# Performance work log

Hardware: AMD Instinct MI355X
Metric: run time of the kernel (lower is better)

Reference implementation:

```python
import jax, jax.numpy as jnp
import numpy as np

N, T, K, R, DK = 4096, 8, 4, 8, 64
S = 2   # slot_dim (2D coords)
B = 20  # noise samples (hardcoded in original forward)


def _conv1d(x, w, b, pad):
    # x: [batch, Cin, L], w: [Cout, Cin, ks] (torch Conv1d layout == OIH)
    y = jax.lax.conv_general_dilated(x, w, (1,), [(pad, pad)],
                                     dimension_numbers=('NCH', 'OIH', 'NCH'))
    return y + b[None, :, None]


def setup_inputs() -> dict:
    key = jax.random.key(0)
    ks = iter(jax.random.split(key, 40))
    r = lambda shape, s=0.1: jax.random.normal(next(ks), shape, jnp.float32) * s
    return dict(
        obs=r((1, S, N, T), 1.0),
        obs_vel=r((1, S, N, T), 1.0),
        noise=r((B, 2, 1, 1), 1.0),
        wq_rule=r((S * T, DK)), bq_rule=r((DK,)),
        wq_ctx=r((2 * S * T, DK)), bq_ctx=r((DK,)),
        wk_ctx=r((2 * S * T, DK)), bk_ctx=r((DK,)),
        rule_emb=r((R, DK), 1.0),
        w_noise=r((R,), 1.0), w_indiv=r((R,), 1.0), w_social=r((R,), 1.0),
        sp_w=r((R, S, S * (K + 1), 3)), sp_b=r((R, S)),
        spr_w=r((R, S, S * (K + 1), 1)), spr_b=r((R, S)),
        tp_w=r((R, 12, T, 3)), tp_b=r((R, 12)),
        tpr_w=r((R, 12, T, 1)), tpr_b=r((R, 12)),
        spi_w=r((R, S, S, 3)), spi_b=r((R, S)),
        spir_w=r((R, S, S, 1)), spir_b=r((R, S)),
        tpi_w=r((R, 12, T, 3)), tpi_b=r((R, 12)),
        tpir_w=r((R, 12, T, 1)), tpir_b=r((R, 12)),
    )


def reference(obs, obs_vel, noise, wq_rule, bq_rule, wq_ctx, bq_ctx, wk_ctx, bk_ctx,
              rule_emb, w_noise, w_indiv, w_social,
              sp_w, sp_b, spr_w, spr_b, tp_w, tp_b, tpr_w, tpr_b,
              spi_w, spi_b, spir_w, spir_b, tpi_w, tpi_b, tpir_w, tpir_b):
    # ---- context selection (eval path: topk_onehot) ----
    cat = jnp.concatenate([obs, obs_vel], axis=1)[0]           # [2S, N, T]
    x_ctx = jnp.transpose(cat, (1, 2, 0)).reshape(N, -1)       # [N, T*2S]
    q = x_ctx @ wq_ctx + bq_ctx
    k_ = x_ctx @ wk_ctx + bk_ctx
    attn_ctx = jax.nn.softmax(q @ k_.T, axis=-1)               # [N, N]
    _, ctx_idx = jax.lax.top_k(attn_ctx, K)                    # [N, K]
    # gather == bmm with one-hot [N,N] masks in the original
    ov_node = jnp.transpose(obs_vel[0], (1, 0, 2))             # [N, S, T]
    ctx_vel = ov_node[ctx_idx]                                 # [N, K, S, T]
    ctx_vel = jnp.transpose(ctx_vel, (1, 2, 0, 3)).reshape(1, K * S, N, T)

    # ---- rule selection (hard top-1) ----
    x_rule = jnp.transpose(obs_vel[0], (1, 2, 0)).reshape(N, -1)  # [N, T*S]
    rq = x_rule @ wq_rule + bq_rule
    attn_rule = jax.nn.softmax(rq @ rule_emb.T, axis=-1)       # [N, R]
    rule_mask = jax.nn.one_hot(jnp.argmax(attn_rule, -1), R, dtype=obs.dtype)  # [N, R]

    noise_rep = jnp.tile(noise, (1, K, 1, 1))                  # [B, K*S, 1, 1]

    def rule_fn(wn, wi, ws, p):
        ov = obs_vel + noise * wn                              # [B, S, N, T]
        ov_f = jnp.transpose(ov, (0, 2, 1, 3)).reshape(B * N, S, T)
        cv = ctx_vel + noise_rep * wn                          # [B, K*S, N, T]
        cv_f = jnp.transpose(cv, (0, 2, 1, 3)).reshape(B * N, K * S, T)
        comb = jnp.concatenate([ov_f, cv_f], axis=1)           # [B*N, S*(K+1), T]
        si = jax.nn.relu(_conv1d(ov_f, p['spi_w'], p['spi_b'], 1)) \
             + _conv1d(ov_f, p['spir_w'], p['spir_b'], 0)      # [B*N, S, T]
        ti = jnp.transpose(si, (0, 2, 1))                      # [B*N, T, S]
        indiv = _conv1d(ti, p['tpi_w'], p['tpi_b'], 1) + _conv1d(ti, p['tpir_w'], p['tpir_b'], 0)
        ss = jax.nn.relu(_conv1d(comb, p['sp_w'], p['sp_b'], 1)) \
             + _conv1d(comb, p['spr_w'], p['spr_b'], 0)        # [B*N, S, T]
        ts = jnp.transpose(ss, (0, 2, 1))
        social = _conv1d(ts, p['tp_w'], p['tp_b'], 1) + _conv1d(ts, p['tpr_w'], p['tpr_b'], 0)
        return wi * indiv + ws * social                        # [B*N, 12, S]

    params = dict(sp_w=sp_w, sp_b=sp_b, spr_w=spr_w, spr_b=spr_b,
                  tp_w=tp_w, tp_b=tp_b, tpr_w=tpr_w, tpr_b=tpr_b,
                  spi_w=spi_w, spi_b=spi_b, spir_w=spir_w, spir_b=spir_b,
                  tpi_w=tpi_w, tpi_b=tpi_b, tpir_w=tpir_w, tpir_b=tpir_b)
    preds = jax.vmap(rule_fn)(w_noise, w_indiv, w_social, params)  # [R, B*N, 12, S]
    preds = preds.reshape(R, B, N, 12, S)
    # hard rule dispatch + final permute(0,2,3,1) of the original -> [B, N, 12, S]
    return jnp.einsum('rbnts,nr->bnts', preds, rule_mask)
```

## Files before the change

kernel.cpp:

```cpp
#include <hip/hip_runtime.h>
#include <cstdint>
#include <cstddef>

#define N_   4096
#define T_   8
#define K_   4
#define R_   8
#define DK_  64
#define S_   2
#define B_   20
#define NT_  (N_*T_)

__device__ __forceinline__ unsigned long long mkkey(float v, int col) {
    unsigned u = __float_as_uint(v);
    u = (u & 0x80000000u) ? ~u : (u | 0x80000000u);
    return ((unsigned long long)u << 32) | (unsigned)(~col);
}

#define INS4(t0,t1,t2,t3,keyexpr) do {                                  \
    unsigned long long _k = (keyexpr);                                  \
    if (_k > (t3)) {                                                    \
        bool _g2 = _k > (t2), _g1 = _k > (t1), _g0 = _k > (t0);         \
        (t3) = _g2 ? (t2) : _k;                                         \
        (t2) = _g2 ? (_g1 ? (t1) : _k) : (t2);                          \
        (t1) = _g1 ? (_g0 ? (t0) : _k) : (t1);                          \
        (t0) = _g0 ? _k : (t0);                                         \
    }                                                                   \
} while (0)

__device__ __forceinline__ unsigned long long shfl_xor_u64(unsigned long long v, int m) {
    unsigned lo = (unsigned)v, hi = (unsigned)(v >> 32);
    lo = __shfl_xor(lo, m, 64);
    hi = __shfl_xor(hi, m, 64);
    return ((unsigned long long)hi << 32) | lo;
}

__global__ __launch_bounds__(256) void proj_kernel(
    const float* __restrict__ obs, const float* __restrict__ obsv,
    const float* __restrict__ wq_ctx, const float* __restrict__ bq_ctx,
    const float* __restrict__ wk_ctx, const float* __restrict__ bk_ctx,
    const float* __restrict__ wq_rule, const float* __restrict__ bq_rule,
    const float* __restrict__ rule_emb,
    float* __restrict__ qg, float* __restrict__ kg, int* __restrict__ rid)
{
    int wv = threadIdx.x >> 6, d = threadIdx.x & 63;
    int n = blockIdx.x * 4 + wv;
    __shared__ float xs[4][32];
    if (d < 32) {
        int t = d >> 2, c = d & 3;
        const float* src = (c < 2) ? obs : obsv;
        xs[wv][d] = src[(c & 1) * NT_ + n * T_ + t];
    }
    __syncthreads();
    const float* x = xs[wv];
    float q = bq_ctx[d], k = bk_ctx[d], rq = bq_rule[d];
    #pragma unroll
    for (int i = 0; i < 32; ++i) {
        float xv = x[i];
        q = fmaf(xv, wq_ctx[i*64 + d], q);
        k = fmaf(xv, wk_ctx[i*64 + d], k);
    }
    #pragma unroll
    for (int i = 0; i < 16; ++i) {
        int t = i >> 1, s = i & 1;
        rq = fmaf(x[t*4 + 2 + s], wq_rule[i*64 + d], rq);
    }
    qg[n*64 + d] = q;
    kg[n*64 + d] = k;

    float best = -1e30f; int bestr = 0;
    #pragma unroll
    for (int r = 0; r < 8; ++r) {
        float p = rq * rule_emb[r*64 + d];
        #pragma unroll
        for (int off = 32; off > 0; off >>= 1) p += __shfl_xor(p, off, 64);
        if (p > best) { best = p; bestr = r; }
    }
    if (d == 0) rid[n] = bestr;
}

#define RPB     64
#define CTILE   64
#define NSPLIT  16
#define DPAD    68

__global__ __launch_bounds__(256) void attn_topk_kernel(
    const float* __restrict__ qg, const float* __restrict__ kg,
    unsigned long long* __restrict__ part)
{
    __shared__ float qT[DK_*DPAD];
    __shared__ float kT[DK_*DPAD];

    int tid = threadIdx.x;
    int tx = tid & 15, ty = tid >> 4;
    int rowblk = blockIdx.x >> 4, split = blockIdx.x & 15;
    int row0 = rowblk * RPB;
    int colbase = split * (N_ / NSPLIT);

    #pragma unroll
    for (int i = 0; i < 4; ++i) {
        int chunk = tid + 256*i;
        int row = chunk & 63, dchunk = chunk >> 6;
        float4 v = *(const float4*)(qg + (size_t)(row0 + row)*64 + 4*dchunk);
        qT[(4*dchunk+0)*DPAD + row] = v.x;
        qT[(4*dchunk+1)*DPAD + row] = v.y;
        qT[(4*dchunk+2)*DPAD + row] = v.z;
        qT[(4*dchunk+3)*DPAD + row] = v.w;
    }

    unsigned long long T0a=0,T0b=0,T0c=0,T0d=0;
    unsigned long long T1a=0,T1b=0,T1c=0,T1d=0;
    unsigned long long T2a=0,T2b=0,T2c=0,T2d=0;
    unsigned long long T3a=0,T3b=0,T3c=0,T3d=0;

    for (int tile = 0; tile < (N_/NSPLIT)/CTILE; ++tile) {
        int c0 = colbase + tile * CTILE;
        __syncthreads();
        #pragma unroll
        for (int i = 0; i < 4; ++i) {
            int chunk = tid + 256*i;
            int col = chunk & 63, dchunk = chunk >> 6;
            float4 v = *(const float4*)(kg + (size_t)(c0 + col)*64 + 4*dchunk);
            kT[(4*dchunk+0)*DPAD + col] = v.x;
            kT[(4*dchunk+1)*DPAD + col] = v.y;
            kT[(4*dchunk+2)*DPAD + col] = v.z;
            kT[(4*dchunk+3)*DPAD + col] = v.w;
        }
        __syncthreads();

        float c00=0,c01=0,c02=0,c03=0, c10=0,c11=0,c12=0,c13=0;
        float c20=0,c21=0,c22=0,c23=0, c30=0,c31=0,c32=0,c33=0;

        #pragma unroll 4
        for (int d = 0; d < 64; ++d) {
            float4 a = *(const float4*)(&qT[d*DPAD + 4*ty]);
            float4 b = *(const float4*)(&kT[d*DPAD + 4*tx]);
            c00 = fmaf(a.x, b.x, c00); c01 = fmaf(a.x, b.y, c01);
            c02 = fmaf(a.x, b.z, c02); c03 = fmaf(a.x, b.w, c03);
            c10 = fmaf(a.y, b.x, c10); c11 = fmaf(a.y, b.y, c11);
            c12 = fmaf(a.y, b.z, c12); c13 = fmaf(a.y, b.w, c13);
            c20 = fmaf(a.z, b.x, c20); c21 = fmaf(a.z, b.y, c21);
            c22 = fmaf(a.z, b.z, c22); c23 = fmaf(a.z, b.w, c23);
            c30 = fmaf(a.w, b.x, c30); c31 = fmaf(a.w, b.y, c31);
            c32 = fmaf(a.w, b.z, c32); c33 = fmaf(a.w, b.w, c33);
        }
        int cc = c0 + 4*tx;
        INS4(T0a,T0b,T0c,T0d, mkkey(c00, cc+0));
        INS4(T0a,T0b,T0c,T0d, mkkey(c01, cc+1));
        INS4(T0a,T0b,T0c,T0d, mkkey(c02, cc+2));
        INS4(T0a,T0b,T0c,T0d, mkkey(c03, cc+3));
        INS4(T1a,T1b,T1c,T1d, mkkey(c10, cc+0));
        INS4(T1a,T1b,T1c,T1d, mkkey(c11, cc+1));
        INS4(T1a,T1b,T1c,T1d, mkkey(c12, cc+2));
        INS4(T1a,T1b,T1c,T1d, mkkey(c13, cc+3));
        INS4(T2a,T2b,T2c,T2d, mkkey(c20, cc+0));
        INS4(T2a,T2b,T2c,T2d, mkkey(c21, cc+1));
        INS4(T2a,T2b,T2c,T2d, mkkey(c22, cc+2));
        INS4(T2a,T2b,T2c,T2d, mkkey(c23, cc+3));
        INS4(T3a,T3b,T3c,T3d, mkkey(c30, cc+0));
        INS4(T3a,T3b,T3c,T3d, mkkey(c31, cc+1));
        INS4(T3a,T3b,T3c,T3d, mkkey(c32, cc+2));
        INS4(T3a,T3b,T3c,T3d, mkkey(c33, cc+3));
    }

    #pragma unroll
    for (int m = 1; m < 16; m <<= 1) {
        unsigned long long r0, r1, r2, r3;
        r0 = shfl_xor_u64(T0a, m); r1 = shfl_xor_u64(T0b, m);
        r2 = shfl_xor_u64(T0c, m); r3 = shfl_xor_u64(T0d, m);
        INS4(T0a,T0b,T0c,T0d, r0); INS4(T0a,T0b,T0c,T0d, r1);
        INS4(T0a,T0b,T0c,T0d, r2); INS4(T0a,T0b,T0c,T0d, r3);
        r0 = shfl_xor_u64(T1a, m); r1 = shfl_xor_u64(T1b, m);
        r2 = shfl_xor_u64(T1c, m); r3 = shfl_xor_u64(T1d, m);
        INS4(T1a,T1b,T1c,T1d, r0); INS4(T1a,T1b,T1c,T1d, r1);
        INS4(T1a,T1b,T1c,T1d, r2); INS4(T1a,T1b,T1c,T1d, r3);
        r0 = shfl_xor_u64(T2a, m); r1 = shfl_xor_u64(T2b, m);
        r2 = shfl_xor_u64(T2c, m); r3 = shfl_xor_u64(T2d, m);
        INS4(T2a,T2b,T2c,T2d, r0); INS4(T2a,T2b,T2c,T2d, r1);
        INS4(T2a,T2b,T2c,T2d, r2); INS4(T2a,T2b,T2c,T2d, r3);
        r0 = shfl_xor_u64(T3a, m); r1 = shfl_xor_u64(T3b, m);
        r2 = shfl_xor_u64(T3c, m); r3 = shfl_xor_u64(T3d, m);
        INS4(T3a,T3b,T3c,T3d, r0); INS4(T3a,T3b,T3c,T3d, r1);
        INS4(T3a,T3b,T3c,T3d, r2); INS4(T3a,T3b,T3c,T3d, r3);
    }

    if (tx == 0) {
        unsigned long long* q;
        q = &part[(size_t)((row0 + 4*ty + 0)*NSPLIT + split)*4];
        q[0]=T0a; q[1]=T0b; q[2]=T0c; q[3]=T0d;
        q = &part[(size_t)((row0 + 4*ty + 1)*NSPLIT + split)*4];
        q[0]=T1a; q[1]=T1b; q[2]=T1c; q[3]=T1d;
        q = &part[(size_t)((row0 + 4*ty + 2)*NSPLIT + split)*4];
        q[0]=T2a; q[1]=T2b; q[2]=T2c; q[3]=T2d;
        q = &part[(size_t)((row0 + 4*ty + 3)*NSPLIT + split)*4];
        q[0]=T3a; q[1]=T3b; q[2]=T3c; q[3]=T3d;
    }
}

__global__ __launch_bounds__(256) void merge_kernel(
    const unsigned long long* __restrict__ part, int* __restrict__ cidx)
{
    int n = blockIdx.x * blockDim.x + threadIdx.x;
    if (n >= N_) return;
    unsigned long long m0=0,m1=0,m2=0,m3=0;
    #pragma unroll 8
    for (int j = 0; j < NSPLIT*4; ++j) INS4(m0,m1,m2,m3, part[(size_t)n*NSPLIT*4 + j]);
    cidx[n*4 + 0] = (int)(~((unsigned)(m0 & 0xffffffffull)));
    cidx[n*4 + 1] = (int)(~((unsigned)(m1 & 0xffffffffull)));
    cidx[n*4 + 2] = (int)(~((unsigned)(m2 & 0xffffffffull)));
    cidx[n*4 + 3] = (int)(~((unsigned)(m3 & 0xffffffffull)));
}

#define WST 708

__global__ __launch_bounds__(256) void predict_kernel(
    const float* __restrict__ obsv, const float* __restrict__ noise,
    const float* __restrict__ w_noise, const float* __restrict__ w_indiv,
    const float* __restrict__ w_social,
    const float* __restrict__ sp_w, const float* __restrict__ sp_b,
    const float* __restrict__ spr_w, const float* __restrict__ spr_b,
    const float* __restrict__ tp_w, const float* __restrict__ tp_b,
    const float* __restrict__ tpr_w, const float* __restrict__ tpr_b,
    const float* __restrict__ spi_w, const float* __restrict__ spi_b,
    const float* __restrict__ spir_w, const float* __restrict__ spir_b,
    const float* __restrict__ tpi_w, const float* __restrict__ tpi_b,
    const float* __restrict__ tpir_w, const float* __restrict__ tpir_b,
    const int* __restrict__ rid, const int* __restrict__ cidx,
    float* __restrict__ out)
{
    __shared__ float W[R_*WST];
    __shared__ float nz_s[B_*2];
    __shared__ float wn_s[R_], wi_s[R_], ws_s[R_];
    int tid = threadIdx.x;

    for (int idx = tid; idx < R_*704; idx += 256) {
        int r = idx / 704, o = idx % 704;
        float v;
        if (o < 12)      v = spi_w[r*12 + o];
        else if (o < 16) v = spir_w[r*4 + (o-12)];
        else if (o < 76) v = sp_w[r*60 + (o-16)];
        else if (o < 96) v = spr_w[r*20 + (o-76)];
        else if (o < 192) { int q=o-96;  int t=q/12, co=q%12; v = tpi_w[((r*12+co)*8+t)*3+1] + tpir_w[(r*12+co)*8+t]; }
        else if (o < 288) { int q=o-192; int t=q/12, co=q%12; v = tpi_w[((r*12+co)*8+t)*3+2]; }
        else if (o < 384) { int q=o-288; int t=q/12, co=q%12; v = tpi_w[((r*12+co)*8+t)*3+0]; }
        else if (o < 480) { int q=o-384; int t=q/12, co=q%12; v = tp_w[((r*12+co)*8+t)*3+1] + tpr_w[(r*12+co)*8+t]; }
        else if (o < 576) { int q=o-480; int t=q/12, co=q%12; v = tp_w[((r*12+co)*8+t)*3+2]; }
        else if (o < 672) { int q=o-576; int t=q/12, co=q%12; v = tp_w[((r*12+co)*8+t)*3+0]; }
        else if (o < 674) v = spi_b[r*2 + (o-672)];
        else if (o < 676) v = spir_b[r*2 + (o-674)];
        else if (o < 678) v = sp_b[r*2 + (o-676)];
        else if (o < 680) v = spr_b[r*2 + (o-678)];
        else if (o < 692) v = tpi_b[r*12 + (o-680)] + tpir_b[r*12 + (o-680)];
        else              v = tp_b[r*12 + (o-692)] + tpr_b[r*12 + (o-692)];
        W[r*WST + o] = v;
    }
    if (tid < B_*2)                  nz_s[tid] = noise[tid];
    if (tid >= 64  && tid < 64+R_)   wn_s[tid-64]  = w_noise[tid-64];
    if (tid >= 96  && tid < 96+R_)   wi_s[tid-96]  = w_indiv[tid-96];
    if (tid >= 128 && tid < 128+R_)  ws_s[tid-128] = w_social[tid-128];
    __syncthreads();

    int item = blockIdx.x*256 + tid;
    if (item >= B_*N_) return;
    int n = item / B_, b = item - n*B_;
    int r = rid[n];
    const float* Wr = &W[r*WST];
    float wn = wn_s[r];
    float nz0 = nz_s[b*2+0]*wn, nz1 = nz_s[b*2+1]*wn;

    float x[10][8];
    #pragma unroll
    for (int s = 0; s < 2; ++s) {
        float4 a = *(const float4*)(obsv + s*NT_ + n*8);
        float4 c = *(const float4*)(obsv + s*NT_ + n*8 + 4);
        float nz = s ? nz1 : nz0;
        x[s][0]=a.x+nz; x[s][1]=a.y+nz; x[s][2]=a.z+nz; x[s][3]=a.w+nz;
        x[s][4]=c.x+nz; x[s][5]=c.y+nz; x[s][6]=c.z+nz; x[s][7]=c.w+nz;
    }
    #pragma unroll
    for (int k = 0; k < 4; ++k) {
        int cn = cidx[n*4 + k];
        #pragma unroll
        for (int s = 0; s < 2; ++s) {
            float4 a = *(const float4*)(obsv + s*NT_ + cn*8);
            float4 c = *(const float4*)(obsv + s*NT_ + cn*8 + 4);
            float nz = s ? nz1 : nz0;
            int ch = 2 + k*2 + s;
            x[ch][0]=a.x+nz; x[ch][1]=a.y+nz; x[ch][2]=a.z+nz; x[ch][3]=a.w+nz;
            x[ch][4]=c.x+nz; x[ch][5]=c.y+nz; x[ch][6]=c.z+nz; x[ch][7]=c.w+nz;
        }
    }

    float si[2][8];
    #pragma unroll
    for (int so = 0; so < 2; ++so) {
        float pre[8];
        float bb = Wr[672+so];
        #pragma unroll
        for (int t = 0; t < 8; ++t) pre[t] = bb;
        #pragma unroll
        for (int ci = 0; ci < 2; ++ci) {
            float w0 = Wr[so*6+ci*3+0], w1 = Wr[so*6+ci*3+1], w2 = Wr[so*6+ci*3+2];
            pre[0] += x[ci][0]*w1 + x[ci][1]*w2;
            #pragma unroll
            for (int t = 1; t < 7; ++t) pre[t] += x[ci][t-1]*w0 + x[ci][t]*w1 + x[ci][t+1]*w2;
            pre[7] += x[ci][6]*w0 + x[ci][7]*w1;
        }
        float l0 = Wr[12+so*2+0], l1 = Wr[12+so*2+1];
        float lb = Wr[674+so];
        #pragma unroll
        for (int t = 0; t < 8; ++t)
            si[so][t] = fmaxf(pre[t], 0.f) + lb + x[0][t]*l0 + x[1][t]*l1;
    }

    float ss[2][8];
    #pragma unroll
    for (int so = 0; so < 2; ++so) {
        float pre[8], lin[8];
        float bb = Wr[676+so], lb = Wr[678+so];
        #pragma unroll
        for (int t = 0; t < 8; ++t) { pre[t] = bb; lin[t] = lb; }
        #pragma unroll
        for (int ci = 0; ci < 10; ++ci) {
            float w0 = Wr[16+so*30+ci*3+0], w1 = Wr[16+so*30+ci*3+1], w2 = Wr[16+so*30+ci*3+2];
            float lw = Wr[76+so*10+ci];
            pre[0] += x[ci][0]*w1 + x[ci][1]*w2;
            #pragma unroll
            for (int t = 1; t < 7; ++t) pre[t] += x[ci][t-1]*w0 + x[ci][t]*w1 + x[ci][t+1]*w2;
            pre[7] += x[ci][6]*w0 + x[ci][7]*w1;
            #pragma unroll
            for (int t = 0; t < 8; ++t) lin[t] += x[ci][t]*lw;
        }
        #pragma unroll
        for (int t = 0; t < 8; ++t) ss[so][t] = fmaxf(pre[t], 0.f) + lin[t];
    }

    float i0[12], i1[12], s0a[12], s1a[12];
    #pragma unroll
    for (int co = 0; co < 12; ++co) {
        float bi = Wr[680+co], bs = Wr[692+co];
        i0[co]=bi; i1[co]=bi; s0a[co]=bs; s1a[co]=bs;
    }
    #pragma unroll
    for (int t = 0; t < 8; ++t) {
        float a0 = si[0][t], a1 = si[1][t];
        float b0 = ss[0][t], b1 = ss[1][t];
        #pragma unroll
        for (int co = 0; co < 12; ++co) {
            i0[co]  += a0*Wr[96 +t*12+co] + a1*Wr[192+t*12+co];
            i1[co]  += a1*Wr[96 +t*12+co] + a0*Wr[288+t*12+co];
            s0a[co] += b0*Wr[384+t*12+co] + b1*Wr[480+t*12+co];
            s1a[co] += b1*Wr[384+t*12+co] + b0*Wr[576+t*12+co];
        }
    }

    float wi = wi_s[r], wsoc = ws_s[r];
    float o[24];
    #pragma unroll
    for (int co = 0; co < 12; ++co) {
        o[co*2+0] = wi*i0[co] + wsoc*s0a[co];
        o[co*2+1] = wi*i1[co] + wsoc*s1a[co];
    }
    float* dst = out + (size_t)(b*N_ + n)*24;
    #pragma unroll
    for (int q4 = 0; q4 < 6; ++q4)
        *(float4*)(dst + q4*4) = *(const float4*)(&o[q4*4]);
}

extern "C" void kernel_launch(void* const* d_in, const int* in_sizes, int n_in,
                              void* d_out, int out_size, void* d_ws, size_t ws_size,
                              hipStream_t stream)
{
    const float* obs      = (const float*)d_in[0];
    const float* obsv     = (const float*)d_in[1];
    const float* noise    = (const float*)d_in[2];
    const float* wq_rule  = (const float*)d_in[3];
    const float* bq_rule  = (const float*)d_in[4];
    const float* wq_ctx   = (const float*)d_in[5];
    const float* bq_ctx   = (const float*)d_in[6];
    const float* wk_ctx   = (const float*)d_in[7];
    const float* bk_ctx   = (const float*)d_in[8];
    const float* rule_emb = (const float*)d_in[9];
    const float* w_noise  = (const float*)d_in[10];
    const float* w_indiv  = (const float*)d_in[11];
    const float* w_social = (const float*)d_in[12];
    const float* sp_w  = (const float*)d_in[13];
    const float* sp_b  = (const float*)d_in[14];
    const float* spr_w = (const float*)d_in[15];
    const float* spr_b = (const float*)d_in[16];
    const float* tp_w  = (const float*)d_in[17];
    const float* tp_b  = (const float*)d_in[18];
    const float* tpr_w = (const float*)d_in[19];
    const float* tpr_b = (const float*)d_in[20];
    const float* spi_w  = (const float*)d_in[21];
    const float* spi_b  = (const float*)d_in[22];
    const float* spir_w = (const float*)d_in[23];
    const float* spir_b = (const float*)d_in[24];
    const float* tpi_w  = (const float*)d_in[25];
    const float* tpi_b  = (const float*)d_in[26];
    const float* tpir_w = (const float*)d_in[27];
    const float* tpir_b = (const float*)d_in[28];

    char* ws = (char*)d_ws;
    float* qg = (float*)(ws);
    float* kg = (float*)(ws + 1048576);
    unsigned long long* part = (unsigned long long*)(ws + 2097152);
    int* rid  = (int*)(ws + 4194304);
    int* cidx = (int*)(ws + 4210688);

    hipLaunchKernelGGL(proj_kernel, dim3(N_/4), dim3(256), 0, stream,
        obs, obsv, wq_ctx, bq_ctx, wk_ctx, bk_ctx, wq_rule, bq_rule, rule_emb,
        qg, kg, rid);

    hipLaunchKernelGGL(attn_topk_kernel, dim3((N_/RPB)*NSPLIT), dim3(256), 0, stream,
        qg, kg, part);

    hipLaunchKernelGGL(merge_kernel, dim3(N_/256), dim3(256), 0, stream,
        part, cidx);

    hipLaunchKernelGGL(predict_kernel, dim3((B_*N_)/256), dim3(256), 0, stream,
        obsv, noise, w_noise, w_indiv, w_social,
        sp_w, sp_b, spr_w, spr_b, tp_w, tp_b, tpr_w, tpr_b,
        spi_w, spi_b, spir_w, spir_b, tpi_w, tpi_b, tpir_w, tpir_b,
        rid, cidx, (float*)d_out);
}
```

Measured before the change: 213.9 us.

## Widen attention tile to 4x8 per thread and prepack rule weights once

Result: faster. 204.4 us (-4.4%).

```diff
diff --git a/kernel.cpp b/kernel.cpp
--- a/kernel.cpp
+++ b/kernel.cpp
@@ -80,32 +80,33 @@
 }
 
 #define RPB     64
-#define CTILE   64
-#define NSPLIT  16
-#define DPAD    68
+#define CTILE   128
+#define NSPLIT  8
+#define QST     68
+#define KST2    132
 
 __global__ __launch_bounds__(256) void attn_topk_kernel(
     const float* __restrict__ qg, const float* __restrict__ kg,
     unsigned long long* __restrict__ part)
 {
-    __shared__ float qT[DK_*DPAD];
-    __shared__ float kT[DK_*DPAD];
+    __shared__ float qT[DK_*QST];
+    __shared__ float kT[DK_*KST2];
 
     int tid = threadIdx.x;
     int tx = tid & 15, ty = tid >> 4;
-    int rowblk = blockIdx.x >> 4, split = blockIdx.x & 15;
+    int rowblk = blockIdx.x >> 3, split = blockIdx.x & 7;
     int row0 = rowblk * RPB;
     int colbase = split * (N_ / NSPLIT);
 
     #pragma unroll
     for (int i = 0; i < 4; ++i) {
         int chunk = tid + 256*i;
-        int row = chunk & 63, dchunk = chunk >> 6;
-        float4 v = *(const float4*)(qg + (size_t)(row0 + row)*64 + 4*dchunk);
-        qT[(4*dchunk+0)*DPAD + row] = v.x;
-        qT[(4*dchunk+1)*DPAD + row] = v.y;
-        qT[(4*dchunk+2)*DPAD + row] = v.z;
-        qT[(4*dchunk+3)*DPAD + row] = v.w;
+        int row = chunk & 63, dc = chunk >> 6;
+        float4 v = *(const float4*)(qg + (size_t)(row0 + row)*64 + 4*dc);
+        qT[(4*dc+0)*QST + row] = v.x;
+        qT[(4*dc+1)*QST + row] = v.y;
+        qT[(4*dc+2)*QST + row] = v.z;
+        qT[(4*dc+3)*QST + row] = v.w;
     }
 
     unsigned long long T0a=0,T0b=0,T0c=0,T0d=0;
@@ -117,50 +118,52 @@
         int c0 = colbase + tile * CTILE;
         __syncthreads();
         #pragma unroll
-        for (int i = 0; i < 4; ++i) {
+        for (int i = 0; i < 8; ++i) {
             int chunk = tid + 256*i;
-            int col = chunk & 63, dchunk = chunk >> 6;
-            float4 v = *(const float4*)(kg + (size_t)(c0 + col)*64 + 4*dchunk);
-            kT[(4*dchunk+0)*DPAD + col] = v.x;
-            kT[(4*dchunk+1)*DPAD + col] = v.y;
-            kT[(4*dchunk+2)*DPAD + col] = v.z;
-            kT[(4*dchunk+3)*DPAD + col] = v.w;
+            int col = chunk & 127, dc = chunk >> 7;
+            float4 v = *(const float4*)(kg + (size_t)(c0 + col)*64 + 4*dc);
+            kT[(4*dc+0)*KST2 + col] = v.x;
+            kT[(4*dc+1)*KST2 + col] = v.y;
+            kT[(4*dc+2)*KST2 + col] = v.z;
+            kT[(4*dc+3)*KST2 + col] = v.w;
         }
         __syncthreads();
 
-        float c00=0,c01=0,c02=0,c03=0, c10=0,c11=0,c12=0,c13=0;
-        float c20=0,c21=0,c22=0,c23=0, c30=0,c31=0,c32=0,c33=0;
-
-        #pragma unroll 4
+        float acc[4][8];
+        #pragma unroll
+        for (int i = 0; i < 4; ++i)
+            #pragma unroll
+            for (int j = 0; j < 8; ++j) acc[i][j] = 0.f;
+
+        #pragma unroll 2
         for (int d = 0; d < 64; ++d) {
-            float4 a = *(const float4*)(&qT[d*DPAD + 4*ty]);
-            float4 b = *(const float4*)(&kT[d*DPAD + 4*tx]);
-            c00 = fmaf(a.x, b.x, c00); c01 = fmaf(a.x, b.y, c01);
-            c02 = fmaf(a.x, b.z, c02); c03 = fmaf(a.x, b.w, c03);
-            c10 = fmaf(a.y, b.x, c10); c11 = fmaf(a.y, b.y, c11);
-            c12 = fmaf(a.y, b.z, c12); c13 = fmaf(a.y, b.w, c13);
-            c20 = fmaf(a.z, b.x, c20); c21 = fmaf(a.z, b.y, c21);
-            c22 = fmaf(a.z, b.z, c22); c23 = fmaf(a.z, b.w, c23);
-            c30 = fmaf(a.w, b.x, c30); c31 = fmaf(a.w, b.y, c31);
-            c32 = fmaf(a.w, b.z, c32); c33 = fmaf(a.w, b.w, c33);
-        }
-        int cc = c0 + 4*tx;
-        INS4(T0a,T0b,T0c,T0d, mkkey(c00, cc+0));
-        INS4(T0a,T0b,T0c,T0d, mkkey(c01, cc+1));
-        INS4(T0a,T0b,T0c,T0d, mkkey(c02, cc+2));
-        INS4(T0a,T0b,T0c,T0d, mkkey(c03, cc+3));
-        INS4(T1a,T1b,T1c,T1d, mkkey(c10, cc+0));
-        INS4(T1a,T1b,T1c,T1d, mkkey(c11, cc+1));
-        INS4(T1a,T1b,T1c,T1d, mkkey(c12, cc+2));
-        INS4(T1a,T1b,T1c,T1d, mkkey(c13, cc+3));
-        INS4(T2a,T2b,T2c,T2d, mkkey(c20, cc+0));
-        INS4(T2a,T2b,T2c,T2d, mkkey(c21, cc+1));
-        INS4(T2a,T2b,T2c,T2d, mkkey(c22, cc+2));
-        INS4(T2a,T2b,T2c,T2d, mkkey(c23, cc+3));
-        INS4(T3a,T3b,T3c,T3d, mkkey(c30, cc+0));
-        INS4(T3a,T3b,T3c,T3d, mkkey(c31, cc+1));
-        INS4(T3a,T3b,T3c,T3d, mkkey(c32, cc+2));
-        INS4(T3a,T3b,T3c,T3d, mkkey(c33, cc+3));
+            float4 a  = *(const float4*)(&qT[d*QST + 4*ty]);
+            float4 b0 = *(const float4*)(&kT[d*KST2 + 4*tx]);
+            float4 b1 = *(const float4*)(&kT[d*KST2 + 64 + 4*tx]);
+            float av[4] = {a.x, a.y, a.z, a.w};
+            float bv[8] = {b0.x, b0.y, b0.z, b0.w, b1.x, b1.y, b1.z, b1.w};
+            #pragma unroll
+            for (int i = 0; i < 4; ++i)
+                #pragma unroll
+                for (int j = 0; j < 8; ++j)
+                    acc[i][j] = fmaf(av[i], bv[j], acc[i][j]);
+        }
+        int ccA = c0 + 4*tx, ccB = c0 + 64 + 4*tx;
+        #define ROW8(t0,t1,t2,t3,i) do {                         \
+            INS4(t0,t1,t2,t3, mkkey(acc[i][0], ccA+0));          \
+            INS4(t0,t1,t2,t3, mkkey(acc[i][1], ccA+1));          \
+            INS4(t0,t1,t2,t3, mkkey(acc[i][2], ccA+2));          \
+            INS4(t0,t1,t2,t3, mkkey(acc[i][3], ccA+3));          \
+            INS4(t0,t1,t2,t3, mkkey(acc[i][4], ccB+0));          \
+            INS4(t0,t1,t2,t3, mkkey(acc[i][5], ccB+1));          \
+            INS4(t0,t1,t2,t3, mkkey(acc[i][6], ccB+2));          \
+            INS4(t0,t1,t2,t3, mkkey(acc[i][7], ccB+3));          \
+        } while (0)
+        ROW8(T0a,T0b,T0c,T0d, 0);
+        ROW8(T1a,T1b,T1c,T1d, 1);
+        ROW8(T2a,T2b,T2c,T2d, 2);
+        ROW8(T3a,T3b,T3c,T3d, 3);
+        #undef ROW8
     }
 
     #pragma unroll
@@ -213,10 +216,7 @@
 
 #define WST 708
 
-__global__ __launch_bounds__(256) void predict_kernel(
-    const float* __restrict__ obsv, const float* __restrict__ noise,
-    const float* __restrict__ w_noise, const float* __restrict__ w_indiv,
-    const float* __restrict__ w_social,
+__global__ __launch_bounds__(256) void prep_kernel(
     const float* __restrict__ sp_w, const float* __restrict__ sp_b,
     const float* __restrict__ spr_w, const float* __restrict__ spr_b,
     const float* __restrict__ tp_w, const float* __restrict__ tp_b,
@@ -225,16 +225,10 @@
     const float* __restrict__ spir_w, const float* __restrict__ spir_b,
     const float* __restrict__ tpi_w, const float* __restrict__ tpi_b,
     const float* __restrict__ tpir_w, const float* __restrict__ tpir_b,
-    const int* __restrict__ rid, const int* __restrict__ cidx,
-    float* __restrict__ out)
-{
-    __shared__ float W[R_*WST];
-    __shared__ float nz_s[B_*2];
-    __shared__ float wn_s[R_], wi_s[R_], ws_s[R_];
-    int tid = threadIdx.x;
-
-    for (int idx = tid; idx < R_*704; idx += 256) {
-        int r = idx / 704, o = idx % 704;
+    float* __restrict__ Wpk)
+{
+    int r = blockIdx.x;
+    for (int o = threadIdx.x; o < 704; o += 256) {
         float v;
         if (o < 12)      v = spi_w[r*12 + o];
         else if (o < 16) v = spir_w[r*4 + (o-12)];
@@ -252,7 +246,27 @@
         else if (o < 680) v = spr_b[r*2 + (o-678)];
         else if (o < 692) v = tpi_b[r*12 + (o-680)] + tpir_b[r*12 + (o-680)];
         else              v = tp_b[r*12 + (o-692)] + tpr_b[r*12 + (o-692)];
-        W[r*WST + o] = v;
+        Wpk[r*WST + o] = v;
+    }
+}
+
+__global__ __launch_bounds__(256) void predict_kernel(
+    const float* __restrict__ obsv, const float* __restrict__ noise,
+    const float* __restrict__ w_noise, const float* __restrict__ w_indiv,
+    const float* __restrict__ w_social,
+    const float* __restrict__ Wpk,
+    const int* __restrict__ rid, const int* __restrict__ cidx,
+    float* __restrict__ out)
+{
+    __shared__ __align__(16) float W[R_*WST];
+    __shared__ float nz_s[B_*2];
+    __shared__ float wn_s[R_], wi_s[R_], ws_s[R_];
+    int tid = threadIdx.x;
+
+    {
+        const float4* src = (const float4*)Wpk;
+        float4* dst = (float4*)W;
+        for (int i = tid; i < (R_*WST)/4; i += 256) dst[i] = src[i];
     }
     if (tid < B_*2)                  nz_s[tid] = noise[tid];
     if (tid >= 64  && tid < 64+R_)   wn_s[tid-64]  = w_noise[tid-64];
@@ -337,20 +351,34 @@
 
     float i0[12], i1[12], s0a[12], s1a[12];
     #pragma unroll
-    for (int co = 0; co < 12; ++co) {
-        float bi = Wr[680+co], bs = Wr[692+co];
-        i0[co]=bi; i1[co]=bi; s0a[co]=bs; s1a[co]=bs;
+    for (int g = 0; g < 3; ++g) {
+        float4 bi = *(const float4*)(&Wr[680 + g*4]);
+        float4 bs = *(const float4*)(&Wr[692 + g*4]);
+        i0[g*4+0]=bi.x; i0[g*4+1]=bi.y; i0[g*4+2]=bi.z; i0[g*4+3]=bi.w;
+        i1[g*4+0]=bi.x; i1[g*4+1]=bi.y; i1[g*4+2]=bi.z; i1[g*4+3]=bi.w;
+        s0a[g*4+0]=bs.x; s0a[g*4+1]=bs.y; s0a[g*4+2]=bs.z; s0a[g*4+3]=bs.w;
+        s1a[g*4+0]=bs.x; s1a[g*4+1]=bs.y; s1a[g*4+2]=bs.z; s1a[g*4+3]=bs.w;
     }
     #pragma unroll
     for (int t = 0; t < 8; ++t) {
         float a0 = si[0][t], a1 = si[1][t];
-        float b0 = ss[0][t], b1 = ss[1][t];
-        #pragma unroll
-        for (int co = 0; co < 12; ++co) {
-            i0[co]  += a0*Wr[96 +t*12+co] + a1*Wr[192+t*12+co];
-            i1[co]  += a1*Wr[96 +t*12+co] + a0*Wr[288+t*12+co];
-            s0a[co] += b0*Wr[384+t*12+co] + b1*Wr[480+t*12+co];
-            s1a[co] += b1*Wr[384+t*12+co] + b0*Wr[576+t*12+co];
+        float b0v = ss[0][t], b1v = ss[1][t];
+        #pragma unroll
+        for (int g = 0; g < 3; ++g) {
+            float4 tA = *(const float4*)(&Wr[96  + t*12 + g*4]);
+            float4 tB = *(const float4*)(&Wr[192 + t*12 + g*4]);
+            float4 tC = *(const float4*)(&Wr[288 + t*12 + g*4]);
+            float4 tD = *(const float4*)(&Wr[384 + t*12 + g*4]);
+            float4 tE = *(const float4*)(&Wr[480 + t*12 + g*4]);
+            float4 tF = *(const float4*)(&Wr[576 + t*12 + g*4]);
+            #define UPD(co, C) do {                              \
+                i0[co]  += a0*tA.C + a1*tB.C;                    \
+                i1[co]  += a1*tA.C + a0*tC.C;                    \
+                s0a[co] += b0v*tD.C + b1v*tE.C;                  \
+                s1a[co] += b1v*tD.C + b0v*tF.C;                  \
+            } while (0)
+            UPD(g*4+0, x); UPD(g*4+1, y); UPD(g*4+2, z); UPD(g*4+3, w);
+            #undef UPD
         }
     }
 
@@ -405,8 +433,13 @@
     float* qg = (float*)(ws);
     float* kg = (float*)(ws + 1048576);
     unsigned long long* part = (unsigned long long*)(ws + 2097152);
-    int* rid  = (int*)(ws + 4194304);
-    int* cidx = (int*)(ws + 4210688);
+    int* rid   = (int*)(ws + 3145728);
+    int* cidx  = (int*)(ws + 3162112);
+    float* Wpk = (float*)(ws + 3227648);
+
+    hipLaunchKernelGGL(prep_kernel, dim3(R_), dim3(256), 0, stream,
+        sp_w, sp_b, spr_w, spr_b, tp_w, tp_b, tpr_w, tpr_b,
+        spi_w, spi_b, spir_w, spir_b, tpi_w, tpi_b, tpir_w, tpir_b, Wpk);
 
     hipLaunchKernelGGL(proj_kernel, dim3(N_/4), dim3(256), 0, stream,
         obs, obsv, wq_ctx, bq_ctx, wk_ctx, bk_ctx, wq_rule, bq_rule, rule_emb,
@@ -419,8 +452,6 @@
         part, cidx);
 
     hipLaunchKernelGGL(predict_kernel, dim3((B_*N_)/256), dim3(256), 0, stream,
-        obsv, noise, w_noise, w_indiv, w_social,
-        sp_w, sp_b, spr_w, spr_b, tp_w, tp_b, tpr_w, tpr_b,
-        spi_w, spi_b, spir_w, spir_b, tpi_w, tpi_b, tpir_w, tpir_b,
+        obsv, noise, w_noise, w_indiv, w_social, Wpk,
         rid, cidx, (float*)d_out);
 }
```

## Fold weight packing into proj kernel and top-k merge into predict kernel

Applied to the files above, without the earlier changes.

Measured after the change: 191.5 us. 10.5% less time.

```diff
diff --git a/kernel.cpp b/kernel.cpp
--- a/kernel.cpp
+++ b/kernel.cpp
@@ -35,14 +35,50 @@
     return ((unsigned long long)hi << 32) | lo;
 }
 
-__global__ __launch_bounds__(256) void proj_kernel(
+#define WST 708
+
+__global__ __launch_bounds__(256) void proj_prep_kernel(
     const float* __restrict__ obs, const float* __restrict__ obsv,
     const float* __restrict__ wq_ctx, const float* __restrict__ bq_ctx,
     const float* __restrict__ wk_ctx, const float* __restrict__ bk_ctx,
     const float* __restrict__ wq_rule, const float* __restrict__ bq_rule,
     const float* __restrict__ rule_emb,
-    float* __restrict__ qg, float* __restrict__ kg, int* __restrict__ rid)
+    const float* __restrict__ sp_w, const float* __restrict__ sp_b,
+    const float* __restrict__ spr_w, const float* __restrict__ spr_b,
+    const float* __restrict__ tp_w, const float* __restrict__ tp_b,
+    const float* __restrict__ tpr_w, const float* __restrict__ tpr_b,
+    const float* __restrict__ spi_w, const float* __restrict__ spi_b,
+    const float* __restrict__ spir_w, const float* __restrict__ spir_b,
+    const float* __restrict__ tpi_w, const float* __restrict__ tpi_b,
+    const float* __restrict__ tpir_w, const float* __restrict__ tpir_b,
+    float* __restrict__ qg, float* __restrict__ kg, int* __restrict__ rid,
+    float* __restrict__ Wpk)
 {
+    if (blockIdx.x >= N_/4) {
+        int r = blockIdx.x - N_/4;
+        for (int o = threadIdx.x; o < 704; o += 256) {
+            float v;
+            if (o < 12)      v = spi_w[r*12 + o];
+            else if (o < 16) v = spir_w[r*4 + (o-12)];
+            else if (o < 76) v = sp_w[r*60 + (o-16)];
+            else if (o < 96) v = spr_w[r*20 + (o-76)];
+            else if (o < 192) { int q=o-96;  int t=q/12, co=q%12; v = tpi_w[((r*12+co)*8+t)*3+1] + tpir_w[(r*12+co)*8+t]; }
+            else if (o < 288) { int q=o-192; int t=q/12, co=q%12; v = tpi_w[((r*12+co)*8+t)*3+2]; }
+            else if (o < 384) { int q=o-288; int t=q/12, co=q%12; v = tpi_w[((r*12+co)*8+t)*3+0]; }
+            else if (o < 480) { int q=o-384; int t=q/12, co=q%12; v = tp_w[((r*12+co)*8+t)*3+1] + tpr_w[(r*12+co)*8+t]; }
+            else if (o < 576) { int q=o-480; int t=q/12, co=q%12; v = tp_w[((r*12+co)*8+t)*3+2]; }
+            else if (o < 672) { int q=o-576; int t=q/12, co=q%12; v = tp_w[((r*12+co)*8+t)*3+0]; }
+            else if (o < 674) v = spi_b[r*2 + (o-672)];
+            else if (o < 676) v = spir_b[r*2 + (o-674)];
+            else if (o < 678) v = sp_b[r*2 + (o-676)];
+            else if (o < 680) v = spr_b[r*2 + (o-678)];
+            else if (o < 692) v = tpi_b[r*12 + (o-680)] + tpir_b[r*12 + (o-680)];
+            else              v = tp_b[r*12 + (o-692)] + tpr_b[r*12 + (o-692)];
+            Wpk[r*WST + o] = v;
+        }
+        return;
+    }
+
     int wv = threadIdx.x >> 6, d = threadIdx.x & 63;
     int n = blockIdx.x * 4 + wv;
     __shared__ float xs[4][32];
@@ -197,72 +233,46 @@
     }
 }
 
-__global__ __launch_bounds__(256) void merge_kernel(
-    const unsigned long long* __restrict__ part, int* __restrict__ cidx)
-{
-    int n = blockIdx.x * blockDim.x + threadIdx.x;
-    if (n >= N_) return;
-    unsigned long long m0=0,m1=0,m2=0,m3=0;
-    #pragma unroll 8
-    for (int j = 0; j < NSPLIT*4; ++j) INS4(m0,m1,m2,m3, part[(size_t)n*NSPLIT*4 + j]);
-    cidx[n*4 + 0] = (int)(~((unsigned)(m0 & 0xffffffffull)));
-    cidx[n*4 + 1] = (int)(~((unsigned)(m1 & 0xffffffffull)));
-    cidx[n*4 + 2] = (int)(~((unsigned)(m2 & 0xffffffffull)));
-    cidx[n*4 + 3] = (int)(~((unsigned)(m3 & 0xffffffffull)));
-}
-
-#define WST 708
-
-__global__ __launch_bounds__(256) void predict_kernel(
+__global__ __launch_bounds__(320) void predict_kernel(
     const float* __restrict__ obsv, const float* __restrict__ noise,
     const float* __restrict__ w_noise, const float* __restrict__ w_indiv,
     const float* __restrict__ w_social,
-    const float* __restrict__ sp_w, const float* __restrict__ sp_b,
-    const float* __restrict__ spr_w, const float* __restrict__ spr_b,
-    const float* __restrict__ tp_w, const float* __restrict__ tp_b,
-    const float* __restrict__ tpr_w, const float* __restrict__ tpr_b,
-    const float* __restrict__ spi_w, const float* __restrict__ spi_b,
-    const float* __restrict__ spir_w, const float* __restrict__ spir_b,
-    const float* __restrict__ tpi_w, const float* __restrict__ tpi_b,
-    const float* __restrict__ tpir_w, const float* __restrict__ tpir_b,
-    const int* __restrict__ rid, const int* __restrict__ cidx,
+    const float* __restrict__ Wpk,
+    const int* __restrict__ rid, const unsigned long long* __restrict__ part,
     float* __restrict__ out)
 {
-    __shared__ float W[R_*WST];
+    __shared__ __align__(16) float W[R_*WST];
+    __shared__ int   cidx_s[16][4];
     __shared__ float nz_s[B_*2];
     __shared__ float wn_s[R_], wi_s[R_], ws_s[R_];
     int tid = threadIdx.x;
-
-    for (int idx = tid; idx < R_*704; idx += 256) {
-        int r = idx / 704, o = idx % 704;
-        float v;
-        if (o < 12)      v = spi_w[r*12 + o];
-        else if (o < 16) v = spir_w[r*4 + (o-12)];
-        else if (o < 76) v = sp_w[r*60 + (o-16)];
-        else if (o < 96) v = spr_w[r*20 + (o-76)];
-        else if (o < 192) { int q=o-96;  int t=q/12, co=q%12; v = tpi_w[((r*12+co)*8+t)*3+1] + tpir_w[(r*12+co)*8+t]; }
-        else if (o < 288) { int q=o-192; int t=q/12, co=q%12; v = tpi_w[((r*12+co)*8+t)*3+2]; }
-        else if (o < 384) { int q=o-288; int t=q/12, co=q%12; v = tpi_w[((r*12+co)*8+t)*3+0]; }
-        else if (o < 480) { int q=o-384; int t=q/12, co=q%12; v = tp_w[((r*12+co)*8+t)*3+1] + tpr_w[(r*12+co)*8+t]; }
-        else if (o < 576) { int q=o-480; int t=q/12, co=q%12; v = tp_w[((r*12+co)*8+t)*3+2]; }
-        else if (o < 672) { int q=o-576; int t=q/12, co=q%12; v = tp_w[((r*12+co)*8+t)*3+0]; }
-        else if (o < 674) v = spi_b[r*2 + (o-672)];
-        else if (o < 676) v = spir_b[r*2 + (o-674)];
-        else if (o < 678) v = sp_b[r*2 + (o-676)];
-        else if (o < 680) v = spr_b[r*2 + (o-678)];
-        else if (o < 692) v = tpi_b[r*12 + (o-680)] + tpir_b[r*12 + (o-680)];
-        else              v = tp_b[r*12 + (o-692)] + tpr_b[r*12 + (o-692)];
-        W[r*WST + o] = v;
+    int n0 = blockIdx.x * 16;
+
+    {
+        const float4* src = (const float4*)Wpk;
+        float4* dst = (float4*)W;
+        for (int i = tid; i < (R_*WST)/4; i += 320) dst[i] = src[i];
     }
     if (tid < B_*2)                  nz_s[tid] = noise[tid];
     if (tid >= 64  && tid < 64+R_)   wn_s[tid-64]  = w_noise[tid-64];
     if (tid >= 96  && tid < 96+R_)   wi_s[tid-96]  = w_indiv[tid-96];
     if (tid >= 128 && tid < 128+R_)  ws_s[tid-128] = w_social[tid-128];
+
+    if (tid >= 160 && tid < 176) {
+        int n = n0 + (tid - 160);
+        unsigned long long m0=0,m1=0,m2=0,m3=0;
+        const unsigned long long* p = &part[(size_t)n*NSPLIT*4];
+        #pragma unroll 8
+        for (int j = 0; j < NSPLIT*4; ++j) INS4(m0,m1,m2,m3, p[j]);
+        cidx_s[tid-160][0] = (int)(~((unsigned)(m0 & 0xffffffffull)));
+        cidx_s[tid-160][1] = (int)(~((unsigned)(m1 & 0xffffffffull)));
+        cidx_s[tid-160][2] = (int)(~((unsigned)(m2 & 0xffffffffull)));
+        cidx_s[tid-160][3] = (int)(~((unsigned)(m3 & 0xffffffffull)));
+    }
     __syncthreads();
 
-    int item = blockIdx.x*256 + tid;
-    if (item >= B_*N_) return;
-    int n = item / B_, b = item - n*B_;
+    int n_local = tid / 20, b = tid - n_local * 20;
+    int n = n0 + n_local;
     int r = rid[n];
     const float* Wr = &W[r*WST];
     float wn = wn_s[r];
@@ -279,7 +289,7 @@
     }
     #pragma unroll
     for (int k = 0; k < 4; ++k) {
-        int cn = cidx[n*4 + k];
+        int cn = cidx_s[n_local][k];
         #pragma unroll
         for (int s = 0; s < 2; ++s) {
             float4 a = *(const float4*)(obsv + s*NT_ + cn*8);
@@ -337,20 +347,34 @@
 
     float i0[12], i1[12], s0a[12], s1a[12];
     #pragma unroll
-    for (int co = 0; co < 12; ++co) {
-        float bi = Wr[680+co], bs = Wr[692+co];
-        i0[co]=bi; i1[co]=bi; s0a[co]=bs; s1a[co]=bs;
+    for (int g = 0; g < 3; ++g) {
+        float4 bi = *(const float4*)(&Wr[680 + g*4]);
+        float4 bs = *(const float4*)(&Wr[692 + g*4]);
+        i0[g*4+0]=bi.x; i0[g*4+1]=bi.y; i0[g*4+2]=bi.z; i0[g*4+3]=bi.w;
+        i1[g*4+0]=bi.x; i1[g*4+1]=bi.y; i1[g*4+2]=bi.z; i1[g*4+3]=bi.w;
+        s0a[g*4+0]=bs.x; s0a[g*4+1]=bs.y; s0a[g*4+2]=bs.z; s0a[g*4+3]=bs.w;
+        s1a[g*4+0]=bs.x; s1a[g*4+1]=bs.y; s1a[g*4+2]=bs.z; s1a[g*4+3]=bs.w;
     }
     #pragma unroll
     for (int t = 0; t < 8; ++t) {
         float a0 = si[0][t], a1 = si[1][t];
-        float b0 = ss[0][t], b1 = ss[1][t];
-        #pragma unroll
-        for (int co = 0; co < 12; ++co) {
-            i0[co]  += a0*Wr[96 +t*12+co] + a1*Wr[192+t*12+co];
-            i1[co]  += a1*Wr[96 +t*12+co] + a0*Wr[288+t*12+co];
-            s0a[co] += b0*Wr[384+t*12+co] + b1*Wr[480+t*12+co];
-            s1a[co] += b1*Wr[384+t*12+co] + b0*Wr[576+t*12+co];
+        float b0v = ss[0][t], b1v = ss[1][t];
+        #pragma unroll
+        for (int g = 0; g < 3; ++g) {
+            float4 tA = *(const float4*)(&Wr[96  + t*12 + g*4]);
+            float4 tB = *(const float4*)(&Wr[192 + t*12 + g*4]);
+            float4 tC = *(const float4*)(&Wr[288 + t*12 + g*4]);
+            float4 tD = *(const float4*)(&Wr[384 + t*12 + g*4]);
+            float4 tE = *(const float4*)(&Wr[480 + t*12 + g*4]);
+            float4 tF = *(const float4*)(&Wr[576 + t*12 + g*4]);
+            #define UPD(co, C) do {                              \
+                i0[co]  += a0*tA.C + a1*tB.C;                    \
+                i1[co]  += a1*tA.C + a0*tC.C;                    \
+                s0a[co] += b0v*tD.C + b1v*tE.C;                  \
+                s1a[co] += b1v*tD.C + b0v*tF.C;                  \
+            } while (0)
+            UPD(g*4+0, x); UPD(g*4+1, y); UPD(g*4+2, z); UPD(g*4+3, w);
+            #undef UPD
         }
     }
 
@@ -405,22 +429,19 @@
     float* qg = (float*)(ws);
     float* kg = (float*)(ws + 1048576);
     unsigned long long* part = (unsigned long long*)(ws + 2097152);
-    int* rid  = (int*)(ws + 4194304);
-    int* cidx = (int*)(ws + 4210688);
-
-    hipLaunchKernelGGL(proj_kernel, dim3(N_/4), dim3(256), 0, stream,
+    int* rid   = (int*)(ws + 4194304);
+    float* Wpk = (float*)(ws + 4210688);
+
+    hipLaunchKernelGGL(proj_prep_kernel, dim3(N_/4 + R_), dim3(256), 0, stream,
         obs, obsv, wq_ctx, bq_ctx, wk_ctx, bk_ctx, wq_rule, bq_rule, rule_emb,
-        qg, kg, rid);
+        sp_w, sp_b, spr_w, spr_b, tp_w, tp_b, tpr_w, tpr_b,
+        spi_w, spi_b, spir_w, spir_b, tpi_w, tpi_b, tpir_w, tpir_b,
+        qg, kg, rid, Wpk);
 
     hipLaunchKernelGGL(attn_topk_kernel, dim3((N_/RPB)*NSPLIT), dim3(256), 0, stream,
         qg, kg, part);
 
-    hipLaunchKernelGGL(merge_kernel, dim3(N_/256), dim3(256), 0, stream,
-        part, cidx);
-
-    hipLaunchKernelGGL(predict_kernel, dim3((B_*N_)/256), dim3(256), 0, stream,
-        obsv, noise, w_noise, w_indiv, w_social,
-        sp_w, sp_b, spr_w, spr_b, tp_w, tp_b, tpr_w, tpr_b,
-        spi_w, spi_b, spir_w, spir_b, tpi_w, tpi_b, tpir_w, tpir_b,
-        rid, cidx, (float*)d_out);
-}
+    hipLaunchKernelGGL(predict_kernel, dim3(N_/16), dim3(320), 0, stream,
+        obsv, noise, w_noise, w_indiv, w_social, Wpk,
+        rid, part, (float*)d_out);
+}
```
